# Performance work log

Hardware: AMD Instinct MI355X
Metric: run time of the kernel (lower is better)

Reference implementation:

```python
import jax, jax.numpy as jnp
import numpy as np

B, S, D, H = 2, 2048, 1024, 16
DK = D // H


def setup_inputs() -> dict:
    key = jax.random.key(0)
    ks = jax.random.split(key, 12)
    s = 0.02
    inp = {
        "query": jax.random.normal(ks[0], (B, S, D), jnp.float32),
        "key": jax.random.normal(ks[1], (B, S, D), jnp.float32),
        "value": jax.random.normal(ks[2], (B, S, D), jnp.float32),
        # causal mask, broadcast over heads inside reference
        "mask": jnp.broadcast_to(jnp.tril(jnp.ones((S, S), jnp.int32)), (B, S, S)),
        "Wq": jax.random.normal(ks[3], (D, D), jnp.float32) * s,
        "bq": jnp.zeros((D,), jnp.float32),
        "Wk": jax.random.normal(ks[4], (D, D), jnp.float32) * s,
        "bk": jnp.zeros((D,), jnp.float32),
        "Wv": jax.random.normal(ks[5], (D, D), jnp.float32) * s,
        "bv": jnp.zeros((D,), jnp.float32),
        "Wo": jax.random.normal(ks[6], (D, D), jnp.float32) * s,
        "bo": jnp.zeros((D,), jnp.float32),
    }
    return inp


def reference(query, key, value, mask, Wq, bq, Wk, bk, Wv, bv, Wo, bo):
    b, sq, d = query.shape
    sk = key.shape[1]
    # projections (torch Linear: x @ W.T + b)
    q = (jnp.einsum('bsd,ed->bse', query, Wq) + bq).reshape(b, sq, H, DK).transpose(0, 2, 1, 3)
    k = (jnp.einsum('bsd,ed->bse', key, Wk) + bk).reshape(b, sk, H, DK).transpose(0, 2, 1, 3)
    v = (jnp.einsum('bsd,ed->bse', value, Wv) + bv).reshape(b, sk, H, DK).transpose(0, 2, 1, 3)
    # scaled dot-product attention, full score matrix as in the original
    scores = jnp.einsum('bhqd,bhkd->bhqk', q, k) / jnp.sqrt(jnp.float32(DK))
    scores = jnp.where(mask[:, None, :, :] == 0, jnp.float32(-1e9), scores)
    p_attn = jax.nn.softmax(scores, axis=-1)  # dropout omitted (eval mode)
    x = jnp.einsum('bhqk,bhkd->bhqd', p_attn, v)
    x = x.transpose(0, 2, 1, 3).reshape(b, sq, d)
    return jnp.einsum('bsd,ed->bse', x, Wo) + bo
```

## Files before the change

### kernel.cpp

```cpp
#include <hip/hip_runtime.h>
#include <hip/hip_bf16.h>

typedef __attribute__((ext_vector_type(8))) short short8;
typedef __attribute__((ext_vector_type(4))) short short4v;
typedef __attribute__((ext_vector_type(4))) float f32x4;

__device__ __forceinline__ short f2bf(float x) {
    __hip_bfloat16 h = __float2bfloat16(x);
    return __builtin_bit_cast(short, h);
}

__device__ __forceinline__ float exp2v(float x) {
    float r;
    asm("v_exp_f32 %0, %1" : "=v"(r) : "v"(x));
    return r;
}

__device__ __forceinline__ void gload16(const void* g, void* l) {
    __builtin_amdgcn_global_load_lds(
        (const __attribute__((address_space(1))) void*)g,
        (__attribute__((address_space(3))) void*)l, 16, 0, 0);
}

#define SWZB(row, cb) ((cb) ^ (((row) & 7) << 4))
#define RESCALE_THR 10.0f

__global__ __launch_bounds__(256) void cvt_all_kernel(
    const float* __restrict__ q, const float* __restrict__ k,
    const float* __restrict__ v, const float* __restrict__ wq,
    const float* __restrict__ wk, const float* __restrict__ wv,
    const float* __restrict__ wo, short* __restrict__ dst) {
    size_t i = ((size_t)blockIdx.x * 256 + threadIdx.x) * 8;
    const float* s; size_t si;
    if (i < 12582912) {
        int w = (int)(i >> 22);
        s = (w == 0) ? q : (w == 1) ? k : v;
        si = i & 4194303;
    } else {
        size_t j = i - 12582912;
        int w = (int)(j >> 20);
        s = (w == 0) ? wq : (w == 1) ? wk : (w == 2) ? wv : wo;
        si = j & 1048575;
    }
    float4 a = *(const float4*)(s + si);
    float4 b = *(const float4*)(s + si + 4);
    short8 o;
    o[0] = f2bf(a.x); o[1] = f2bf(a.y); o[2] = f2bf(a.z); o[3] = f2bf(a.w);
    o[4] = f2bf(b.x); o[5] = f2bf(b.y); o[6] = f2bf(b.z); o[7] = f2bf(b.w);
    *(short8*)(dst + i) = o;
}

__global__ __launch_bounds__(256) void proj_gemm_kernel(
    const __hip_bfloat16* __restrict__ ins,
    const __hip_bfloat16* __restrict__ wts,
    const float* __restrict__ b0, const float* __restrict__ b1,
    const float* __restrict__ b2,
    __hip_bfloat16* __restrict__ outs) {
    __shared__ __align__(16) short Al[128 * 64];
    __shared__ __align__(16) short Bl[64 * 64];
    const int lin = blockIdx.x;
    const int logical = ((lin & 7) * 192) + (lin >> 3);
    const int bx = logical & 15;
    const int by = (logical >> 4) & 31;
    const int z  = logical >> 9;
    const char* Ab = (const char*)(ins + (size_t)z * 4194304)
                     + (size_t)by * 128 * 2048;
    const char* Wb = (const char*)(wts + (size_t)z * 1048576)
                     + (size_t)bx * 64 * 2048;
    const float* bias = (z == 0) ? b0 : (z == 1) ? b1 : b2;
    __hip_bfloat16* out = outs + (size_t)z * 4194304;

    const int tid = threadIdx.x, lane = tid & 63, wid = tid >> 6;
    const int lr = lane & 15, lg = lane >> 4;

    f32x4 acc[2][4] = {};
    for (int kt = 0; kt < 16; ++kt) {
#pragma unroll
        for (int i = 0; i < 4; ++i) {
            int slot0 = (wid * 4 + i) * 64;
            int slot = slot0 + lane;
            int row = slot >> 3;
            int cb = (slot & 7) << 4;
            gload16(Ab + (size_t)row * 2048 + (kt << 7) + SWZB(row, cb),
                    (char*)Al + (slot0 << 4));
        }
#pragma unroll
        for (int i = 0; i < 2; ++i) {
            int slot0 = (wid * 2 + i) * 64;
            int slot = slot0 + lane;
            int row = slot >> 3;
            int cb = (slot & 7) << 4;
            gload16(Wb + (size_t)row * 2048 + (kt << 7) + SWZB(row, cb),
                    (char*)Bl + (slot0 << 4));
        }
        __syncthreads();
#pragma unroll
        for (int kk = 0; kk < 2; ++kk) {
            short8 af[2], bw[4];
#pragma unroll
            for (int m = 0; m < 2; ++m) {
                int row = 32 * wid + 16 * m + lr;
                af[m] = *(const short8*)((char*)Al + row * 128 +
                            SWZB(row, kk * 64 + (lg << 4)));
            }
#pragma unroll
            for (int n = 0; n < 4; ++n) {
                int row = 16 * n + lr;
                bw[n] = *(const short8*)((char*)Bl + row * 128 +
                            SWZB(row, kk * 64 + (lg << 4)));
            }
#pragma unroll
            for (int m = 0; m < 2; ++m)
#pragma unroll
                for (int n = 0; n < 4; ++n)
                    acc[m][n] = __builtin_amdgcn_mfma_f32_16x16x32_bf16(
                        af[m], bw[n], acc[m][n], 0, 0, 0);
        }
        __syncthreads();
    }

    if (z == 2) {
        char* tb = (char*)Al;
#pragma unroll
        for (int n = 0; n < 4; ++n) {
            int ce = 16 * n + lr;
            float bb = bias[(bx << 6) + ce];
#pragma unroll
            for (int m = 0; m < 2; ++m) {
                short4v vv;
#pragma unroll
                for (int r = 0; r < 4; ++r) vv[r] = f2bf(acc[m][n][r] + bb);
                int byteoff = (wid << 6) + (m << 5) + (lg << 3);
                *(short4v*)(tb + ce * 256 +
                            (byteoff ^ ((ce & 15) << 4))) = vv;
            }
        }
        __syncthreads();
#pragma unroll
        for (int i = 0; i < 4; ++i) {
            int c = tid + (i << 8);
            int re = c >> 4;
            int pos = c & 15;
            short8 vv = *(const short8*)(tb + re * 256 +
                            ((pos << 4) ^ ((re & 15) << 4)));
            int e = (bx << 6) + re;
            int hh = e >> 6, dk = e & 63;
            int srow = (by << 7) + (pos << 3);
            int bat = srow >> 11, s = srow & 2047;
            *(short8*)((short*)out +
                ((size_t)((bat * 16 + hh) * 64 + dk) << 11) + s) = vv;
        }
        return;
    }

    const float scale = (z == 0) ? 0.125f * 1.44269504f : 1.0f;
#pragma unroll
    for (int n = 0; n < 4; ++n) {
        int col = (bx << 6) + 16 * n + lr;
        float bb = bias[col];
        int hh = col >> 6, dk = col & 63;
#pragma unroll
        for (int m = 0; m < 2; ++m)
#pragma unroll
            for (int r = 0; r < 4; ++r) {
                int row = (by << 7) + (wid << 5) + 16 * m + 4 * lg + r;
                int bat = row >> 11, s = row & 2047;
                out[((size_t)((bat * 16 + hh) * 2048 + s) << 6) + dk] =
                    __float2bfloat16((acc[m][n][r] + bb) * scale);
            }
    }
}

__global__ __launch_bounds__(256) void out_gemm_kernel(
    const __hip_bfloat16* __restrict__ X, const __hip_bfloat16* __restrict__ Wo,
    const float* __restrict__ bias, float* __restrict__ out) {
    __shared__ __align__(16) short Al[64 * 64];
    __shared__ __align__(16) short Bl[64 * 64];
    const int lin = blockIdx.x;
    const int logical = ((lin & 7) * 128) + (lin >> 3);
    const int bx = logical & 15;
    const int by = logical >> 4;
    const char* Ab = (const char*)X + (size_t)by * 64 * 2048;
    const char* Wb = (const char*)Wo + (size_t)bx * 64 * 2048;
    const int tid = threadIdx.x, lane = tid & 63, wid = tid >> 6;
    const int lr = lane & 15, lg = lane >> 4;

    f32x4 acc[4] = {};
    for (int kt = 0; kt < 16; ++kt) {
#pragma unroll
        for (int i = 0; i < 2; ++i) {
            int slot0 = (wid * 2 + i) * 64;
            int slot = slot0 + lane;
            int row = slot >> 3, cb = (slot & 7) << 4;
            gload16(Ab + (size_t)row * 2048 + (kt << 7) + SWZB(row, cb),
                    (char*)Al + (slot0 << 4));
        }
#pragma unroll
        for (int i = 0; i < 2; ++i) {
            int slot0 = (wid * 2 + i) * 64;
            int slot = slot0 + lane;
            int row = slot >> 3, cb = (slot & 7) << 4;
            gload16(Wb + (size_t)row * 2048 + (kt << 7) + SWZB(row, cb),
                    (char*)Bl + (slot0 << 4));
        }
        __syncthreads();
#pragma unroll
        for (int kk = 0; kk < 2; ++kk) {
            short8 af, bw[4];
            {
                int row = (wid << 4) + lr;
                af = *(const short8*)((char*)Al + row * 128 +
                        SWZB(row, kk * 64 + (lg << 4)));
            }
#pragma unroll
            for (int n = 0; n < 4; ++n) {
                int row = 16 * n + lr;
                bw[n] = *(const short8*)((char*)Bl + row * 128 +
                            SWZB(row, kk * 64 + (lg << 4)));
            }
#pragma unroll
            for (int n = 0; n < 4; ++n)
                acc[n] = __builtin_amdgcn_mfma_f32_16x16x32_bf16(
                    af, bw[n], acc[n], 0, 0, 0);
        }
        __syncthreads();
    }

    int col0 = (bx << 6);
    int row0 = (by << 6) + (wid << 4);
#pragma unroll
    for (int n = 0; n < 4; ++n) {
        int col = col0 + 16 * n + lr;
        float bb = bias[col];
#pragma unroll
        for (int r = 0; r < 4; ++r) {
            int row = row0 + 4 * lg + r;
            out[((size_t)row << 10) + col] = acc[n][r] + bb;
        }
    }
}

__global__ __launch_bounds__(512) void attn_kernel(
    const __hip_bfloat16* __restrict__ qb, const __hip_bfloat16* __restrict__ kb,
    const __hip_bfloat16* __restrict__ vtb, __hip_bfloat16* __restrict__ xb) {
    __shared__ __align__(16) char smem[40960];
    const int tid = threadIdx.x, lane = tid & 63, wid = tid >> 6;
    const int ws = wid & 3, kvh = wid >> 2;
    const int lr = lane & 15, lg = lane >> 4;
    const int lin = blockIdx.x;
    const int logical = ((lin & 7) * 64) + (lin >> 3);
    const int px = logical & 15;
    const int h = (logical >> 4) & 15;
    const int b = logical >> 8;
    const size_t hb = (size_t)(b * 16 + h) * (2048 * 64);
    const short* qg = (const short*)qb + hb;
    const short* kg = (const short*)kb + hb;
    const short* vtg = (const short*)vtb + hb;
    char* pw = smem + 32768 + ws * 2048;
    const short8 ones = {16256, 16256, 16256, 16256,
                         16256, 16256, 16256, 16256};
    const int csrc = (lane & 48) | ((lane >> 2) & 12);
    const int srow = tid >> 3, scb = (tid & 7) << 4;
    const int sswz = SWZB(srow, scb);

#pragma unroll 1
    for (int half = 0; half < 2; ++half) {
        const int qt = half ? (31 - px) : px;
        const int q0 = qt << 6;
        const int ntiles = qt + 1;

        short8 qa[2];
        const char* qrow = (const char*)(qg + (size_t)q0 * 64)
                           + (16 * ws + lr) * 128 + (lg << 4);
        qa[0] = *(const short8*)(qrow);
        qa[1] = *(const short8*)(qrow + 64);

        f32x4 o[4] = {};
        f32x4 lacc = {};
        float m = -1e30f;
        const int qcol = q0 + 16 * ws + lr;
        const int qorow = q0 + 16 * ws + 4 * lg;

        {
            gload16((const char*)(kg + (size_t)srow * 64) + sswz,
                    smem + (wid << 10));
            gload16((const char*)(vtg + (size_t)srow * 2048) + sswz,
                    smem + 16384 + (wid << 10));
        }
        int cur = 0;
#pragma unroll 1
        for (int t = 0; t < ntiles; ++t) {
            if (t + 1 < ntiles) {
                const int kv0 = (t + 1) << 6;
                gload16((const char*)(kg + (size_t)(kv0 + srow) * 64) + sswz,
                        smem + ((cur ^ 1) << 13) + (wid << 10));
                gload16((const char*)(vtg + (size_t)srow * 2048 + kv0) + sswz,
                        smem + 16384 + ((cur ^ 1) << 13) + (wid << 10));
                asm volatile("s_waitcnt vmcnt(2)" ::: "memory");
            } else {
                asm volatile("s_waitcnt vmcnt(0)" ::: "memory");
            }
            __builtin_amdgcn_s_barrier();

            const char* Kc = smem + (cur << 13);
            const char* Vc = smem + 16384 + (cur << 13);

            f32x4 sc[2] = {};
            __builtin_amdgcn_s_setprio(1);
#pragma unroll
            for (int kk = 0; kk < 2; ++kk)
#pragma unroll
                for (int n = 0; n < 2; ++n) {
                    int row = 32 * kvh + 16 * n + lr;
                    short8 kf = *(const short8*)(Kc + row * 128 +
                                    SWZB(row, kk * 64 + (lg << 4)));
                    sc[n] = __builtin_amdgcn_mfma_f32_16x16x32_bf16(
                        kf, qa[kk], sc[n], 0, 0, 0);
                }
            __builtin_amdgcn_s_setprio(0);

            if (t == qt) {
                const int kvb = (t << 6) + 32 * kvh;
#pragma unroll
                for (int n = 0; n < 2; ++n)
#pragma unroll
                    for (int r = 0; r < 4; ++r)
                        if (kvb + 16 * n + 4 * lg + r > qcol)
                            sc[n][r] = -1e30f;
            }

            float pm;
            {
                float t0 = fmaxf(fmaxf(sc[0][0], sc[0][1]),
                                 fmaxf(sc[0][2], sc[0][3]));
                float t1 = fmaxf(fmaxf(sc[1][0], sc[1][1]),
                                 fmaxf(sc[1][2], sc[1][3]));
                pm = fmaxf(t0, t1);
                pm = fmaxf(pm, __shfl_xor(pm, 16));
                pm = fmaxf(pm, __shfl_xor(pm, 32));
            }

            if (__any(pm > m + RESCALE_THR)) {
                float mnew = fmaxf(m, pm);
                float corrq = exp2v(m - mnew);
                m = mnew;
#pragma unroll
                for (int r = 0; r < 4; ++r) {
                    float c = __shfl(corrq, csrc + r);
                    lacc[r] *= c;
#pragma unroll
                    for (int nd = 0; nd < 4; ++nd) o[nd][r] *= c;
                }
            }

#pragma unroll
            for (int n = 0; n < 2; ++n)
#pragma unroll
                for (int rr = 0; rr < 2; ++rr) {
                    float p0 = exp2v(sc[n][2 * rr] - m);
                    float p1 = exp2v(sc[n][2 * rr + 1] - m);
                    unsigned w;
                    asm("v_cvt_pk_bf16_f32 %0, %1, %2"
                        : "=v"(w) : "v"(p0), "v"(p1));
                    int bcol = 64 * kvh + 32 * n + 8 * lg + 4 * rr;
                    *(unsigned*)(pw + lr * 128 + SWZB(lr, bcol)) = w;
                }

            __builtin_amdgcn_s_setprio(1);
            {
                short8 pa = *(const short8*)(pw + lr * 128 +
                                SWZB(lr, kvh * 64 + (lg << 4)));
                lacc = __builtin_amdgcn_mfma_f32_16x16x32_bf16(
                    pa, ones, lacc, 0, 0, 0);
#pragma unroll
                for (int nd = 0; nd < 4; ++nd) {
                    int row = 16 * nd + lr;
                    short8 vf = *(const short8*)(Vc + row * 128 +
                                    SWZB(row, kvh * 64 + (lg << 4)));
                    o[nd] = __builtin_amdgcn_mfma_f32_16x16x32_bf16(
                        pa, vf, o[nd], 0, 0, 0);
                }
            }
            __builtin_amdgcn_s_setprio(0);
            __builtin_amdgcn_s_barrier();
            cur ^= 1;
        }

        float* mb = (float*)smem;
        const int mi = ((ws << 6) + lane) * 25;
        float mo[4];
#pragma unroll
        for (int r = 0; r < 4; ++r) mo[r] = __shfl(m, csrc + r);
        if (kvh == 1) {
#pragma unroll
            for (int r = 0; r < 4; ++r) {
                mb[mi + r] = mo[r];
                mb[mi + 4 + r] = lacc[r];
            }
#pragma unroll
            for (int nd = 0; nd < 4; ++nd)
#pragma unroll
                for (int r = 0; r < 4; ++r)
                    mb[mi + 8 + nd * 4 + r] = o[nd][r];
        }
        asm volatile("s_waitcnt lgkmcnt(0)" ::: "memory");
        __builtin_amdgcn_s_barrier();
        if (kvh == 0) {
#pragma unroll
            for (int r = 0; r < 4; ++r) {
                float mB = mb[mi + r];
                float lB = mb[mi + 4 + r];
                float M = fmaxf(mo[r], mB);
                float cA = exp2v(mo[r] - M);
                float cB = exp2v(mB - M);
                float inv = 1.0f / (lacc[r] * cA + lB * cB);
                int s = qorow + r;
                size_t rowoff = ((size_t)(b * 2048 + s) << 10) + (h << 6);
#pragma unroll
                for (int nd = 0; nd < 4; ++nd) {
                    float ov = o[nd][r] * cA + mb[mi + 8 + nd * 4 + r] * cB;
                    xb[rowoff + 16 * nd + lr] = __float2bfloat16(ov * inv);
                }
            }
        }
        __builtin_amdgcn_s_barrier();
    }
}

extern "C" void kernel_launch(void* const* d_in, const int* in_sizes, int n_in,
                              void* d_out, int out_size, void* d_ws, size_t ws_size,
                              hipStream_t stream) {
    const float* query = (const float*)d_in[0];
    const float* key_  = (const float*)d_in[1];
    const float* value = (const float*)d_in[2];
    const float* Wq = (const float*)d_in[4];
    const float* bq = (const float*)d_in[5];
    const float* Wk = (const float*)d_in[6];
    const float* bk = (const float*)d_in[7];
    const float* Wv = (const float*)d_in[8];
    const float* bv = (const float*)d_in[9];
    const float* Wo = (const float*)d_in[10];
    const float* bo = (const float*)d_in[11];

    __hip_bfloat16* ws    = (__hip_bfloat16*)d_ws;
    __hip_bfloat16* in_b  = ws;
    __hip_bfloat16* w_b   = ws + 12582912;
    __hip_bfloat16* qkv_b = ws + 16777216;
    __hip_bfloat16* x_b   = ws;

    cvt_all_kernel<<<8192, 256, 0, stream>>>(query, key_, value,
                                             Wq, Wk, Wv, Wo, (short*)in_b);
    proj_gemm_kernel<<<1536, 256, 0, stream>>>(in_b, w_b, bq, bk, bv, qkv_b);
    attn_kernel<<<512, 512, 0, stream>>>(qkv_b, qkv_b + 4194304,
                                         qkv_b + 8388608, x_b);
    out_gemm_kernel<<<1024, 256, 0, stream>>>(x_b, w_b + 3145728, bo,
                                              (float*)d_out);
}
```

Measured before the change: 104.0 us.

## Process two 64-row query tiles per attention block to share K/V loads

Each attention block now handles two adjacent query tiles (128 query rows), and every wave computes two 16-row query groups against each staged K/V tile. K and V fragments read from shared memory are reused across both query groups, and each KV tile is fetched once for 128 queries instead of 64. The grid is halved to 256 blocks. In exchange the block does more causal-masked work on the diagonal, uses more registers and shared memory, and runs fewer blocks, which may cost occupancy and load balance.

```diff
diff --git a/kernel.cpp b/kernel.cpp
--- a/kernel.cpp
+++ b/kernel.cpp
@@ -243,20 +243,20 @@
 __global__ __launch_bounds__(512) void attn_kernel(
     const __hip_bfloat16* __restrict__ qb, const __hip_bfloat16* __restrict__ kb,
     const __hip_bfloat16* __restrict__ vtb, __hip_bfloat16* __restrict__ xb) {
-    __shared__ __align__(16) char smem[40960];
+    __shared__ __align__(16) char smem[49152];
     const int tid = threadIdx.x, lane = tid & 63, wid = tid >> 6;
-    const int ws = wid & 3, kvh = wid >> 2;
+    const int qs = wid >> 2, ws = (wid >> 1) & 1, kvh = wid & 1;
     const int lr = lane & 15, lg = lane >> 4;
     const int lin = blockIdx.x;
-    const int logical = ((lin & 7) * 64) + (lin >> 3);
-    const int px = logical & 15;
-    const int h = (logical >> 4) & 15;
-    const int b = logical >> 8;
+    const int logical = ((lin & 7) * 32) + (lin >> 3);
+    const int j = logical & 7;
+    const int h = (logical >> 3) & 15;
+    const int b = logical >> 7;
     const size_t hb = (size_t)(b * 16 + h) * (2048 * 64);
-    const short* qg = (const short*)qb + hb;
+    const short* qg_ = (const short*)qb + hb;
     const short* kg = (const short*)kb + hb;
     const short* vtg = (const short*)vtb + hb;
-    char* pw = smem + 32768 + ws * 2048;
+    char* pw = smem + 32768 + (wid << 11);
     const short8 ones = {16256, 16256, 16256, 16256,
                          16256, 16256, 16256, 16256};
     const int csrc = (lane & 48) | ((lane >> 2) & 12);
@@ -264,22 +264,28 @@
     const int sswz = SWZB(srow, scb);
 
 #pragma unroll 1
-    for (int half = 0; half < 2; ++half) {
-        const int qt = half ? (31 - px) : px;
-        const int q0 = qt << 6;
-        const int ntiles = qt + 1;
-
-        short8 qa[2];
-        const char* qrow = (const char*)(qg + (size_t)q0 * 64)
-                           + (16 * ws + lr) * 128 + (lg << 4);
-        qa[0] = *(const short8*)(qrow);
-        qa[1] = *(const short8*)(qrow + 64);
-
-        f32x4 o[4] = {};
-        f32x4 lacc = {};
-        float m = -1e30f;
-        const int qcol = q0 + 16 * ws + lr;
-        const int qorow = q0 + 16 * ws + 4 * lg;
+    for (int pass = 0; pass < 2; ++pass) {
+        const int qtbase = pass ? (30 - 2 * j) : (2 * j);
+        const int ntiles = pass ? (32 - 2 * j) : (2 * j + 2);
+        const int qtw = qtbase + qs;
+
+        short8 qa[2][2];
+        const char* qbase = (const char*)(qg_ +
+            (size_t)(qtw * 64 + 32 * ws) * 64);
+#pragma unroll
+        for (int qg2 = 0; qg2 < 2; ++qg2)
+#pragma unroll
+            for (int kk = 0; kk < 2; ++kk)
+                qa[qg2][kk] = *(const short8*)(qbase + (16 * qg2 + lr) * 128 +
+                                               kk * 64 + (lg << 4));
+
+        f32x4 o[2][4] = {};
+        f32x4 lacc[2] = {};
+        float m[2] = {-1e30f, -1e30f};
+        int qcol[2];
+#pragma unroll
+        for (int qg2 = 0; qg2 < 2; ++qg2)
+            qcol[qg2] = qtw * 64 + 32 * ws + 16 * qg2 + lr;
 
         {
             gload16((const char*)(kg + (size_t)srow * 64) + sswz,
@@ -305,80 +311,98 @@
             const char* Kc = smem + (cur << 13);
             const char* Vc = smem + 16384 + (cur << 13);
 
-            f32x4 sc[2] = {};
+            f32x4 sc[2][2] = {};
             __builtin_amdgcn_s_setprio(1);
 #pragma unroll
             for (int kk = 0; kk < 2; ++kk)
 #pragma unroll
                 for (int n = 0; n < 2; ++n) {
-                    int row = 32 * kvh + 16 * n + lr;
+                    int row = (kvh << 5) + 16 * n + lr;
                     short8 kf = *(const short8*)(Kc + row * 128 +
                                     SWZB(row, kk * 64 + (lg << 4)));
-                    sc[n] = __builtin_amdgcn_mfma_f32_16x16x32_bf16(
-                        kf, qa[kk], sc[n], 0, 0, 0);
+#pragma unroll
+                    for (int qg2 = 0; qg2 < 2; ++qg2)
+                        sc[qg2][n] = __builtin_amdgcn_mfma_f32_16x16x32_bf16(
+                            kf, qa[qg2][kk], sc[qg2][n], 0, 0, 0);
                 }
             __builtin_amdgcn_s_setprio(0);
 
-            if (t == qt) {
-                const int kvb = (t << 6) + 32 * kvh;
+            if (t >= qtw) {
+                const int kvt = (t << 6) + (kvh << 5);
+#pragma unroll
+                for (int qg2 = 0; qg2 < 2; ++qg2)
+#pragma unroll
+                    for (int n = 0; n < 2; ++n)
+#pragma unroll
+                        for (int r = 0; r < 4; ++r)
+                            if (kvt + 16 * n + 4 * lg + r > qcol[qg2])
+                                sc[qg2][n][r] = -1e30f;
+            }
+
+            float pm[2];
+#pragma unroll
+            for (int qg2 = 0; qg2 < 2; ++qg2) {
+                float t0 = fmaxf(fmaxf(sc[qg2][0][0], sc[qg2][0][1]),
+                                 fmaxf(sc[qg2][0][2], sc[qg2][0][3]));
+                float t1 = fmaxf(fmaxf(sc[qg2][1][0], sc[qg2][1][1]),
+                                 fmaxf(sc[qg2][1][2], sc[qg2][1][3]));
+                float p = fmaxf(t0, t1);
+                p = fmaxf(p, __shfl_xor(p, 16));
+                p = fmaxf(p, __shfl_xor(p, 32));
+                pm[qg2] = p;
+            }
+
+            if (__any((pm[0] > m[0] + RESCALE_THR) |
+                      (pm[1] > m[1] + RESCALE_THR))) {
+#pragma unroll
+                for (int qg2 = 0; qg2 < 2; ++qg2) {
+                    float mnew = fmaxf(m[qg2], pm[qg2]);
+                    float corrq = exp2v(m[qg2] - mnew);
+                    m[qg2] = mnew;
+#pragma unroll
+                    for (int r = 0; r < 4; ++r) {
+                        float c = __shfl(corrq, csrc + r);
+                        lacc[qg2][r] *= c;
+#pragma unroll
+                        for (int nd = 0; nd < 4; ++nd) o[qg2][nd][r] *= c;
+                    }
+                }
+            }
+
+#pragma unroll
+            for (int qg2 = 0; qg2 < 2; ++qg2)
 #pragma unroll
                 for (int n = 0; n < 2; ++n)
 #pragma unroll
-                    for (int r = 0; r < 4; ++r)
-                        if (kvb + 16 * n + 4 * lg + r > qcol)
-                            sc[n][r] = -1e30f;
-            }
-
-            float pm;
-            {
-                float t0 = fmaxf(fmaxf(sc[0][0], sc[0][1]),
-                                 fmaxf(sc[0][2], sc[0][3]));
-                float t1 = fmaxf(fmaxf(sc[1][0], sc[1][1]),
-                                 fmaxf(sc[1][2], sc[1][3]));
-                pm = fmaxf(t0, t1);
-                pm = fmaxf(pm, __shfl_xor(pm, 16));
-                pm = fmaxf(pm, __shfl_xor(pm, 32));
-            }
-
-            if (__any(pm > m + RESCALE_THR)) {
-                float mnew = fmaxf(m, pm);
-                float corrq = exp2v(m - mnew);
-                m = mnew;
-#pragma unroll
-                for (int r = 0; r < 4; ++r) {
-                    float c = __shfl(corrq, csrc + r);
-                    lacc[r] *= c;
-#pragma unroll
-                    for (int nd = 0; nd < 4; ++nd) o[nd][r] *= c;
-                }
-            }
-
-#pragma unroll
-            for (int n = 0; n < 2; ++n)
-#pragma unroll
-                for (int rr = 0; rr < 2; ++rr) {
-                    float p0 = exp2v(sc[n][2 * rr] - m);
-                    float p1 = exp2v(sc[n][2 * rr + 1] - m);
-                    unsigned w;
-                    asm("v_cvt_pk_bf16_f32 %0, %1, %2"
-                        : "=v"(w) : "v"(p0), "v"(p1));
-                    int bcol = 64 * kvh + 32 * n + 8 * lg + 4 * rr;
-                    *(unsigned*)(pw + lr * 128 + SWZB(lr, bcol)) = w;
-                }
+                    for (int rr = 0; rr < 2; ++rr) {
+                        float p0 = exp2v(sc[qg2][n][2 * rr] - m[qg2]);
+                        float p1 = exp2v(sc[qg2][n][2 * rr + 1] - m[qg2]);
+                        unsigned w;
+                        asm("v_cvt_pk_bf16_f32 %0, %1, %2"
+                            : "=v"(w) : "v"(p0), "v"(p1));
+                        int bcol = qg2 * 64 + 32 * n + 8 * lg + 4 * rr;
+                        *(unsigned*)(pw + lr * 128 + SWZB(lr, bcol)) = w;
+                    }
 
             __builtin_amdgcn_s_setprio(1);
             {
-                short8 pa = *(const short8*)(pw + lr * 128 +
-                                SWZB(lr, kvh * 64 + (lg << 4)));
-                lacc = __builtin_amdgcn_mfma_f32_16x16x32_bf16(
-                    pa, ones, lacc, 0, 0, 0);
+                short8 pa[2];
+#pragma unroll
+                for (int qg2 = 0; qg2 < 2; ++qg2) {
+                    pa[qg2] = *(const short8*)(pw + lr * 128 +
+                                  SWZB(lr, qg2 * 64 + (lg << 4)));
+                    lacc[qg2] = __builtin_amdgcn_mfma_f32_16x16x32_bf16(
+                        pa[qg2], ones, lacc[qg2], 0, 0, 0);
+                }
 #pragma unroll
                 for (int nd = 0; nd < 4; ++nd) {
                     int row = 16 * nd + lr;
                     short8 vf = *(const short8*)(Vc + row * 128 +
-                                    SWZB(row, kvh * 64 + (lg << 4)));
-                    o[nd] = __builtin_amdgcn_mfma_f32_16x16x32_bf16(
-                        pa, vf, o[nd], 0, 0, 0);
+                                    SWZB(row, (kvh << 6) + (lg << 4)));
+#pragma unroll
+                    for (int qg2 = 0; qg2 < 2; ++qg2)
+                        o[qg2][nd] = __builtin_amdgcn_mfma_f32_16x16x32_bf16(
+                            pa[qg2], vf, o[qg2][nd], 0, 0, 0);
                 }
             }
             __builtin_amdgcn_s_setprio(0);
@@ -387,43 +411,47 @@
         }
 
         float* mb = (float*)smem;
-        const int mi = ((ws << 6) + lane) * 25;
-        float mo[4];
-#pragma unroll
-        for (int r = 0; r < 4; ++r) mo[r] = __shfl(m, csrc + r);
-        if (kvh == 1) {
-#pragma unroll
-            for (int r = 0; r < 4; ++r) {
-                mb[mi + r] = mo[r];
-                mb[mi + 4 + r] = lacc[r];
-            }
-#pragma unroll
-            for (int nd = 0; nd < 4; ++nd)
-#pragma unroll
-                for (int r = 0; r < 4; ++r)
-                    mb[mi + 8 + nd * 4 + r] = o[nd][r];
-        }
-        asm volatile("s_waitcnt lgkmcnt(0)" ::: "memory");
-        __builtin_amdgcn_s_barrier();
-        if (kvh == 0) {
-#pragma unroll
-            for (int r = 0; r < 4; ++r) {
-                float mB = mb[mi + r];
-                float lB = mb[mi + 4 + r];
-                float M = fmaxf(mo[r], mB);
-                float cA = exp2v(mo[r] - M);
-                float cB = exp2v(mB - M);
-                float inv = 1.0f / (lacc[r] * cA + lB * cB);
-                int s = qorow + r;
-                size_t rowoff = ((size_t)(b * 2048 + s) << 10) + (h << 6);
-#pragma unroll
-                for (int nd = 0; nd < 4; ++nd) {
-                    float ov = o[nd][r] * cA + mb[mi + 8 + nd * 4 + r] * cB;
-                    xb[rowoff + 16 * nd + lr] = __float2bfloat16(ov * inv);
-                }
-            }
-        }
-        __builtin_amdgcn_s_barrier();
+        const int mi = (((qs << 1) | ws) * 64 + lane) * 25;
+#pragma unroll 1
+        for (int qg2 = 0; qg2 < 2; ++qg2) {
+            float mo[4];
+#pragma unroll
+            for (int r = 0; r < 4; ++r) mo[r] = __shfl(m[qg2], csrc + r);
+            if (kvh == 1) {
+#pragma unroll
+                for (int r = 0; r < 4; ++r) {
+                    mb[mi + r] = mo[r];
+                    mb[mi + 4 + r] = lacc[qg2][r];
+                }
+#pragma unroll
+                for (int nd = 0; nd < 4; ++nd)
+#pragma unroll
+                    for (int r = 0; r < 4; ++r)
+                        mb[mi + 8 + nd * 4 + r] = o[qg2][nd][r];
+            }
+            asm volatile("s_waitcnt lgkmcnt(0)" ::: "memory");
+            __builtin_amdgcn_s_barrier();
+            if (kvh == 0) {
+#pragma unroll
+                for (int r = 0; r < 4; ++r) {
+                    float mB = mb[mi + r];
+                    float lB = mb[mi + 4 + r];
+                    float M = fmaxf(mo[r], mB);
+                    float cA = exp2v(mo[r] - M);
+                    float cB = exp2v(mB - M);
+                    float inv = 1.0f / (lacc[qg2][r] * cA + lB * cB);
+                    int s = qtw * 64 + 32 * ws + 16 * qg2 + 4 * lg + r;
+                    size_t rowoff = ((size_t)(b * 2048 + s) << 10) + (h << 6);
+#pragma unroll
+                    for (int nd = 0; nd < 4; ++nd) {
+                        float ov = o[qg2][nd][r] * cA +
+                                   mb[mi + 8 + nd * 4 + r] * cB;
+                        xb[rowoff + 16 * nd + lr] = __float2bfloat16(ov * inv);
+                    }
+                }
+            }
+            __builtin_amdgcn_s_barrier();
+        }
     }
 }
 
@@ -451,7 +479,7 @@
     cvt_all_kernel<<<8192, 256, 0, stream>>>(query, key_, value,
                                              Wq, Wk, Wv, Wo, (short*)in_b);
     proj_gemm_kernel<<<1536, 256, 0, stream>>>(in_b, w_b, bq, bk, bv, qkv_b);
-    attn_kernel<<<512, 512, 0, stream>>>(qkv_b, qkv_b + 4194304,
+    attn_kernel<<<256, 512, 0, stream>>>(qkv_b, qkv_b + 4194304,
                                          qkv_b + 8388608, x_b);
     out_gemm_kernel<<<1024, 256, 0, stream>>>(x_b, w_b + 3145728, bo,
                                               (float*)d_out);
```

Measured after the change: 183.6 us. +76.4%, slower.
